# Performance work log

Hardware: AMD Instinct MI355X
Metric: run time of the kernel (lower is better)

## Reference

```python
import jax, jax.numpy as jnp
import numpy as np

GROUP_NORM_EPSILON = 1e-06
NUM_GROUPS = 32


def group_norm(x, gamma, beta, num_groups, eps):
    # x: [B, H, W, C]; normalize over (H, W, C//G) within each group.
    B, H, W, C = x.shape
    xg = x.reshape(B, H, W, num_groups, C // num_groups)
    mean = jnp.mean(xg, axis=(1, 2, 4), keepdims=True)
    var = jnp.mean(jnp.square(xg - mean), axis=(1, 2, 4), keepdims=True)
    xn = (xg - mean) * jax.lax.rsqrt(var + eps)
    return xn.reshape(B, H, W, C) * gamma + beta


def setup_inputs() -> dict:
    key = jax.random.key(0)
    ks = jax.random.split(key, 6)
    B, H, W, C = 4, 64, 64, 512
    scale = 1.0 / np.sqrt(C)
    return {
        "inputs": jax.random.normal(ks[0], (B, H, W, C), dtype=jnp.float32),
        "gamma": jnp.ones((C,), dtype=jnp.float32),
        "beta": jnp.zeros((C,), dtype=jnp.float32),
        "Wq": jax.random.normal(ks[1], (C, C), dtype=jnp.float32) * scale,
        "bq": jnp.zeros((C,), dtype=jnp.float32),
        "Wk": jax.random.normal(ks[2], (C, C), dtype=jnp.float32) * scale,
        "bk": jnp.zeros((C,), dtype=jnp.float32),
        "Wv": jax.random.normal(ks[3], (C, C), dtype=jnp.float32) * scale,
        "bv": jnp.zeros((C,), dtype=jnp.float32),
        "Wo": jax.random.normal(ks[4], (C, C), dtype=jnp.float32) * scale,
        "bo": jnp.zeros((C,), dtype=jnp.float32),
    }


def reference(inputs, gamma, beta, Wq, bq, Wk, bk, Wv, bv, Wo, bo):
    B, H, W, C = inputs.shape
    N = H * W
    h = group_norm(inputs, gamma, beta, NUM_GROUPS, GROUP_NORM_EPSILON)
    hf = h.reshape(B, N, C)  # flatten spatial: [B, N, C]
    q = hf @ Wq + bq
    k = hf @ Wk + bk
    v = hf @ Wv + bv
    # full spatial self-attention: [B, N, N]
    scores = jnp.einsum("bnc,bmc->bnm", q, k) * (C ** -0.5)
    attn = jax.nn.softmax(scores, axis=-1)
    out = jnp.einsum("bnm,bmc->bnc", attn, v)
    out = out @ Wo + bo
    return out.reshape(B, H, W, C) + inputs
```

## Files before the change

kernel.cpp:

```cpp
#include <hip/hip_runtime.h>
#include <hip/hip_bf16.h>

using bf16 = __hip_bfloat16;
using u16  = unsigned short;
typedef __attribute__((ext_vector_type(8))) short s16x8;
typedef __attribute__((ext_vector_type(4))) float f32x4;

__device__ __forceinline__ float b2f(u16 u){
  union{unsigned u; float f;} c; c.u = ((unsigned)u)<<16; return c.f;
}
__device__ __forceinline__ u16 f2b(float f){
  __hip_bfloat16 h = __float2bfloat16(f);
  return *reinterpret_cast<u16*>(&h);
}

#define GLDS16(g, l_) __builtin_amdgcn_global_load_lds( \
    (const __attribute__((address_space(1))) unsigned int*)(g), \
    (__attribute__((address_space(3))) unsigned int*)(l_), 16, 0, 0)

__global__ __launch_bounds__(512) void gn_kernel(const float* __restrict__ x,
    const float* __restrict__ gamma, const float* __restrict__ beta,
    bf16* __restrict__ h)
{
  const int b = blockIdx.x >> 5, g = blockIdx.x & 31;
  const int t = threadIdx.x;
  const size_t base = (size_t)b*4096*512 + (size_t)g*16;
  float sum = 0.f, sq = 0.f;
  for (int i = 0; i < 8; i++){
    const float* p = x + base + (size_t)(i*512 + t)*512;
    #pragma unroll
    for (int j = 0; j < 4; j++){
      f32x4 v = *(const f32x4*)(p + j*4);
      #pragma unroll
      for (int e = 0; e < 4; e++){ sum += v[e]; sq += v[e]*v[e]; }
    }
  }
  __shared__ float red[16];
  for (int o = 32; o > 0; o >>= 1){ sum += __shfl_xor(sum, o); sq += __shfl_xor(sq, o); }
  const int w = t >> 6, l = t & 63;
  if (l == 0){ red[w] = sum; red[8 + w] = sq; }
  __syncthreads();
  if (t == 0){
    float a = 0.f, bb = 0.f;
    for (int i = 0; i < 8; i++){ a += red[i]; bb += red[8 + i]; }
    red[0] = a; red[8] = bb;
  }
  __syncthreads();
  const float inv_n = 1.f/65536.f;
  const float mean = red[0]*inv_n;
  const float var  = red[8]*inv_n - mean*mean;
  const float rstd = rsqrtf(var + 1e-6f);
  float ga[16], be[16];
  #pragma unroll
  for (int j = 0; j < 16; j++){
    ga[j] = gamma[g*16 + j];
    be[j] = beta [g*16 + j];
  }
  u16* hp = (u16*)h;
  for (int i = 0; i < 8; i++){
    const float* p = x + base + (size_t)(i*512 + t)*512;
    u16* q = hp + base + (size_t)(i*512 + t)*512;
    s16x8 o0, o1;
    #pragma unroll
    for (int j = 0; j < 4; j++){
      f32x4 v = *(const f32x4*)(p + j*4);
      #pragma unroll
      for (int e = 0; e < 4; e++){
        int c = j*4 + e;
        u16 r = f2b((v[e] - mean)*rstd*ga[c] + be[c]);
        if (c < 8) o0[c] = (short)r; else o1[c - 8] = (short)r;
      }
    }
    *(s16x8*)q = o0; *(s16x8*)(q + 8) = o1;
  }
}

struct W4 { const float* p[4]; };
__global__ __launch_bounds__(256) void transpose_w4(W4 srcs, bf16* __restrict__ dst)
{
  __shared__ float tile[64][65];
  const float* in = srcs.p[blockIdx.z];
  u16* out = (u16*)dst + (size_t)blockIdx.z*512*512;
  const int tr = blockIdx.y*64, tc = blockIdx.x*64;
  const int t = threadIdx.x;
  #pragma unroll
  for (int i = 0; i < 16; i++){
    int idx = i*256 + t, r = idx >> 6, c = idx & 63;
    tile[r][c] = in[(size_t)(tr + r)*512 + tc + c];
  }
  __syncthreads();
  #pragma unroll
  for (int i = 0; i < 16; i++){
    int idx = i*256 + t, r = idx >> 6, c = idx & 63;
    out[(size_t)(tc + r)*512 + tr + c] = f2b(tile[c][r]);
  }
}

__global__ __launch_bounds__(256) void transpose_v(const u16* __restrict__ qkv,
    bf16* __restrict__ vT)
{
  __shared__ u16 tile[64][72];
  const u16* in = qkv + 1024 + (size_t)blockIdx.z*4096*1536;
  u16* out = (u16*)vT + (size_t)blockIdx.z*512*4096;
  const int tr = blockIdx.y*64, tc = blockIdx.x*64;
  const int t = threadIdx.x;
  #pragma unroll
  for (int i = 0; i < 16; i++){
    int idx = i*256 + t, r = idx >> 6, c = idx & 63;
    tile[r][c] = in[(size_t)(tr + r)*1536 + tc + c];
  }
  __syncthreads();
  #pragma unroll
  for (int i = 0; i < 16; i++){
    int idx = i*256 + t, r = idx >> 6, c = idx & 63;
    out[(size_t)(tc + r)*4096 + tr + c] = tile[c][r];
  }
}

template<int EPI, typename OutT>
__global__ __launch_bounds__(256) void gemm_bt(
    const u16* __restrict__ A, int lda, long sA,
    const u16* __restrict__ Bt, int ldb, long sB,
    OutT* __restrict__ Cmat, int ldc, long sC,
    int K, float scale,
    const float* __restrict__ b0, const float* __restrict__ b1,
    const float* __restrict__ b2, const float* __restrict__ res)
{
  __shared__ u16 As[128*64];
  __shared__ u16 Bs[128*64];
  const int t = threadIdx.x, l = t & 63, w = t >> 6;
  const int wr = w >> 1, wc = w & 1;
  int bx = blockIdx.x, by = blockIdx.y;
  {
    const int gx = gridDim.x, nb = gx * gridDim.y;
    if ((nb & 7) == 0){
      int lin = by*gx + bx;
      int s = (lin & 7)*(nb >> 3) + (lin >> 3);
      bx = s % gx; by = s / gx;
    }
  }
  const int m0 = by * 128, n0 = bx * 128;
  const u16* Au  = A  + (size_t)blockIdx.z * sA;
  const u16* Btu = Bt + (size_t)blockIdx.z * sB;

  f32x4 acc[4][4];
  #pragma unroll
  for (int m = 0; m < 4; m++)
    #pragma unroll
    for (int n = 0; n < 4; n++) acc[m][n] = (f32x4){0.f,0.f,0.f,0.f};

  const int srow = l >> 3;
  const int scol = ((l & 7) ^ srow) * 8;
  const int xorv = (l & 7) << 4;
  const int nkt = K >> 6;
  for (int kt = 0; kt < nkt; ++kt){
    const int k0 = kt << 6;
    #pragma unroll
    for (int j = 0; j < 4; j++){
      const int chunk = w*4 + j;
      const int row = chunk*8 + srow;
      GLDS16(Au  + (size_t)(m0 + row)*lda + k0 + scol, &As[chunk*512]);
      GLDS16(Btu + (size_t)(n0 + row)*ldb + k0 + scol, &Bs[chunk*512]);
    }
    __syncthreads();
    #pragma unroll
    for (int kk = 0; kk < 2; kk++){
      const int kbyte = (kk*64 + (l >> 4)*16) ^ xorv;
      s16x8 af[4], bff[4];
      #pragma unroll
      for (int m = 0; m < 4; m++)
        af[m]  = *(const s16x8*)((const char*)As + (wr*64 + m*16 + (l & 15))*128 + kbyte);
      #pragma unroll
      for (int n = 0; n < 4; n++)
        bff[n] = *(const s16x8*)((const char*)Bs + (wc*64 + n*16 + (l & 15))*128 + kbyte);
      #pragma unroll
      for (int m = 0; m < 4; m++)
        #pragma unroll
        for (int n = 0; n < 4; n++)
          acc[m][n] = __builtin_amdgcn_mfma_f32_16x16x32_bf16(af[m], bff[n], acc[m][n], 0, 0, 0);
    }
    __syncthreads();
  }
  const int lc = l & 15, lr4 = (l >> 4)*4;
  OutT* Cz = Cmat + (size_t)blockIdx.z * sC;
  #pragma unroll
  for (int n = 0; n < 4; n++){
    const int col = n0 + wc*64 + n*16 + lc;
    float bv = 0.f;
    if (EPI & 8){
      const float* bp = (col < 512) ? b0 : (col < 1024 ? b1 : b2);
      bv = bp[col & 511];
    } else if (EPI & 1){
      bv = b0[col];
    }
    #pragma unroll
    for (int m = 0; m < 4; m++){
      const int rowb = m0 + wr*64 + m*16 + lr4;
      #pragma unroll
      for (int r = 0; r < 4; r++){
        float v = acc[m][n][r];
        if (EPI & 2) v *= scale;
        v += bv;
        const size_t off = (size_t)(rowb + r)*ldc + col;
        if (EPI & 4) v += res[off];
        if constexpr (__is_same(OutT, float)) Cz[off] = v;
        else ((u16*)Cz)[off] = f2b(v);
      }
    }
  }
}

__global__ __launch_bounds__(512) void pv_fused(
    const u16* __restrict__ S, const u16* __restrict__ vT,
    bf16* __restrict__ ao, int batched, int batch0)
{
  __shared__ u16 Bs[256*64];
  __shared__ u16 Ps[64*64];
  __shared__ float lsArr[64];
  const int t = threadIdx.x, l = t & 63, w = t >> 6;
  int batch, mt, half;
  if (batched){
    const int lin = blockIdx.x, x = lin & 7, s = lin >> 3;
    batch = x >> 1; mt = (s >> 1)*2 + (x & 1); half = s & 1;
  } else { batch = batch0; mt = blockIdx.x >> 1; half = blockIdx.x & 1; }
  const int m0 = mt*64, c0 = half*256;
  const u16* Sb  = S  + (size_t)batch*4096*4096;
  const u16* vTb = vT + (size_t)batch*512*4096 + (size_t)c0*4096;
  u16* aob = (u16*)ao + (size_t)batch*4096*512;

  f32x4 acc[4][2];
  #pragma unroll
  for (int m = 0; m < 4; m++)
    #pragma unroll
    for (int n = 0; n < 2; n++) acc[m][n] = (f32x4){0.f,0.f,0.f,0.f};

  const int srow = l >> 3, lane8 = l & 7;
  const int scol = (lane8 ^ srow) * 8;
  const int xorv = lane8 << 4;
  const int r_loc = w*8 + srow;
  const int smaddr = r_loc*128 + ((lane8*16) ^ (srow << 4));
  float lsumrow = 0.f;

  const u16* Srow = Sb + (size_t)(m0 + r_loc)*4096 + lane8*8;

  #pragma unroll
  for (int j = 0; j < 4; j++){
    const int chunk = w*4 + j;
    const int row = chunk*8 + srow;
    GLDS16(vTb + (size_t)row*4096 + scol, &Bs[chunk*512]);
  }
  s16x8 S_cur = *(const s16x8*)Srow;

  for (int kt = 0; kt < 64; ++kt){
    const int ktn = (kt < 63) ? kt + 1 : 63;
    s16x8 S_next = *(const s16x8*)(Srow + ktn*64);

    float rs = 0.f;
    s16x8 pb;
    #pragma unroll
    for (int j = 0; j < 8; j++){
      const float pvv = exp2f(fminf(b2f((u16)S_cur[j]), 100.f));
      rs += pvv;
      pb[j] = (short)f2b(pvv);
    }
    rs += __shfl_xor(rs, 1); rs += __shfl_xor(rs, 2); rs += __shfl_xor(rs, 4);
    lsumrow += rs;

    *(s16x8*)((char*)Ps + smaddr) = pb;

    asm volatile("s_waitcnt lgkmcnt(0)" ::: "memory");
    __builtin_amdgcn_sched_barrier(0);
    asm volatile("s_waitcnt vmcnt(1)" ::: "memory");
    __builtin_amdgcn_sched_barrier(0);
    __builtin_amdgcn_s_barrier();

    #pragma unroll
    for (int kk = 0; kk < 2; kk++){
      const int kbyte = (kk*64 + (l >> 4)*16) ^ xorv;
      s16x8 pa[4], bf2[2];
      #pragma unroll
      for (int m = 0; m < 4; m++)
        pa[m] = *(const s16x8*)((const char*)Ps + (m*16 + (l & 15))*128 + kbyte);
      #pragma unroll
      for (int n = 0; n < 2; n++)
        bf2[n] = *(const s16x8*)((const char*)Bs + (w*32 + n*16 + (l & 15))*128 + kbyte);
      #pragma unroll
      for (int m = 0; m < 4; m++)
        #pragma unroll
        for (int n = 0; n < 2; n++)
          acc[m][n] = __builtin_amdgcn_mfma_f32_16x16x32_bf16(pa[m], bf2[n], acc[m][n], 0, 0, 0);
    }

    __builtin_amdgcn_sched_barrier(0);
    __builtin_amdgcn_s_barrier();
    __builtin_amdgcn_sched_barrier(0);

    #pragma unroll
    for (int j = 0; j < 4; j++){
      const int chunk = w*4 + j;
      const int row = chunk*8 + srow;
      GLDS16(vTb + (size_t)row*4096 + ktn*64 + scol, &Bs[chunk*512]);
    }
    S_cur = S_next;
  }

  if (lane8 == 0) lsArr[r_loc] = lsumrow;
  __syncthreads();
  #pragma unroll
  for (int m = 0; m < 4; m++){
    const f32x4 lq = *(const f32x4*)&lsArr[m*16 + (l >> 4)*4];
    #pragma unroll
    for (int r = 0; r < 4; r++){
      const float inv = 1.f / lq[r];
      const int row = m0 + m*16 + (l >> 4)*4 + r;
      #pragma unroll
      for (int n = 0; n < 2; n++){
        const int col = c0 + w*32 + n*16 + (l & 15);
        aob[(size_t)row*512 + col] = f2b(acc[m][n][r] * inv);
      }
    }
  }
}

extern "C" void kernel_launch(void* const* d_in, const int* in_sizes, int n_in,
                              void* d_out, int out_size, void* d_ws, size_t ws_size,
                              hipStream_t stream)
{
  (void)in_sizes; (void)n_in; (void)out_size;
  const float* x     = (const float*)d_in[0];
  const float* gamma = (const float*)d_in[1];
  const float* beta  = (const float*)d_in[2];
  const float* Wq = (const float*)d_in[3]; const float* bq = (const float*)d_in[4];
  const float* Wk = (const float*)d_in[5]; const float* bk = (const float*)d_in[6];
  const float* Wv = (const float*)d_in[7]; const float* bv = (const float*)d_in[8];
  const float* Wo = (const float*)d_in[9]; const float* bo = (const float*)d_in[10];
  float* out = (float*)d_out;

  const int B = 4, N = 4096, C = 512;
  const long NC = (long)N*C;
  const float scl2 = 0.04419417382415922f * 1.4426950408889634f;

  char* p0 = (char*)d_ws;
  auto align = [](size_t b){ return (b + 255) & ~(size_t)255; };
  const size_t sz_h   = align((size_t)B*NC*2);
  const size_t sz_w   = align((size_t)4*C*C*2);
  const size_t sz_qkvF= align((size_t)B*N*1536*2);
  const size_t sz_vTF = align((size_t)B*NC*2);
  const size_t sz_aoF = align((size_t)B*NC*2);
  const size_t sz_SF  = align((size_t)B*N*N*2);
  const size_t need_full = sz_h + sz_w + sz_qkvF + sz_vTF + sz_aoF + sz_SF;

  bf16* h    = (bf16*)p0;
  bf16* wAll = (bf16*)(p0 + sz_h);
  char* pv   = p0 + sz_h + sz_w;

  gn_kernel<<<dim3(B*32), dim3(512), 0, stream>>>(x, gamma, beta, h);
  W4 ws4; ws4.p[0] = Wq; ws4.p[1] = Wk; ws4.p[2] = Wv; ws4.p[3] = Wo;
  transpose_w4<<<dim3(8, 8, 4), 256, 0, stream>>>(ws4, wAll);
  bf16* woT = wAll + (size_t)3*C*C;

  if (ws_size >= need_full){
    bf16* qkv = (bf16*)pv;
    bf16* vT  = (bf16*)(pv + sz_qkvF);
    bf16* ao  = (bf16*)(pv + sz_qkvF + sz_vTF);
    bf16* S   = (bf16*)(pv + sz_qkvF + sz_vTF + sz_aoF);

    gemm_bt<8, bf16><<<dim3(12, 128, 1), 256, 0, stream>>>(
        (const u16*)h, C, 0, (const u16*)wAll, C, 0, qkv, 1536, 0,
        C, 1.f, bq, bk, bv, nullptr);
    transpose_v<<<dim3(8, 64, B), 256, 0, stream>>>((const u16*)qkv, vT);
    gemm_bt<2, bf16><<<dim3(32, 32, B), 256, 0, stream>>>(
        (const u16*)qkv, 1536, (long)N*1536, (const u16*)qkv + 512, 1536, (long)N*1536,
        S, N, (long)N*N, C, scl2, nullptr, nullptr, nullptr, nullptr);
    pv_fused<<<dim3(512), 512, 0, stream>>>(
        (const u16*)S, (const u16*)vT, ao, 1, 0);
    gemm_bt<5, float><<<dim3(4, 128, 1), 256, 0, stream>>>(
        (const u16*)ao, C, 0, (const u16*)woT, C, 0, out, C, 0,
        C, 1.f, bo, nullptr, nullptr, x);
  } else {
    const size_t sz_qkv1 = align((size_t)N*1536*2);
    const size_t sz_vT1  = align((size_t)NC*2);
    const size_t sz_ao1  = align((size_t)NC*2);
    bf16* qkv = (bf16*)pv;
    bf16* vT  = (bf16*)(pv + sz_qkv1);
    bf16* ao  = (bf16*)(pv + sz_qkv1 + sz_vT1);
    bf16* S   = (bf16*)(pv + sz_qkv1 + sz_vT1 + sz_ao1);
    for (int b = 0; b < B; b++){
      const u16* hb = (const u16*)h + (size_t)b*NC;
      gemm_bt<8, bf16><<<dim3(12, 32, 1), 256, 0, stream>>>(
          hb, C, 0, (const u16*)wAll, C, 0, qkv, 1536, 0,
          C, 1.f, bq, bk, bv, nullptr);
      transpose_v<<<dim3(8, 64, 1), 256, 0, stream>>>((const u16*)qkv, vT);
      gemm_bt<2, bf16><<<dim3(32, 32, 1), 256, 0, stream>>>(
          (const u16*)qkv, 1536, 0, (const u16*)qkv + 512, 1536, 0,
          S, N, 0, C, scl2, nullptr, nullptr, nullptr, nullptr);
      pv_fused<<<dim3(128), 512, 0, stream>>>(
          (const u16*)S, (const u16*)vT, ao, 0, b);
      gemm_bt<5, float><<<dim3(4, 32, 1), 256, 0, stream>>>(
          (const u16*)ao, C, 0, (const u16*)woT, C, 0, out + (size_t)b*NC, C, 0,
          C, 1.f, bo, nullptr, nullptr, x + (size_t)b*NC);
    }
  }
}
```

Measured before the change: 401.4 us.

## Add 256x256-tile pipelined GEMM kernel for QKV projection and QK^T scores

Adds a new gemm256 kernel that uses 512 threads and 256x256 output tiles, with double-buffered LDS staging through global_load_lds, an XOR swizzle and a phased schedule that interleaves MFMA with async loads. It also remaps block indices for L2 locality. The QKV projection and the score GEMM now use it in place of the 128-tile gemm_bt. The larger tiles aim to raise arithmetic intensity and overlap loads with compute, at the cost of higher register and LDS pressure and fewer blocks (the QKV grid shrinks to 384 blocks).

```diff
diff --git a/kernel.cpp b/kernel.cpp
--- a/kernel.cpp
+++ b/kernel.cpp
@@ -208,6 +208,141 @@
       }
     }
   }
+}
+
+template<int EPI, typename OutT>
+__global__ __launch_bounds__(512, 2) void gemm256(
+    const u16* __restrict__ A, int lda, long sA,
+    const u16* __restrict__ Bt, int ldb, long sB,
+    OutT* __restrict__ Cmat, int ldc, long sC,
+    int K, float scale,
+    const float* __restrict__ b0, const float* __restrict__ b1,
+    const float* __restrict__ b2, const float* __restrict__ res)
+{
+  __shared__ u16 L[2][2][2][256*32];
+  const int t = threadIdx.x, l = t & 63, w = t >> 3 >> 3;
+  const int wm = w >> 2, wn = w & 3;
+  int bx = blockIdx.x, by = blockIdx.y;
+  {
+    const int gx = gridDim.x, nb = gx * gridDim.y;
+    if ((nb & 7) == 0){
+      int lin = by*gx + bx;
+      int s = (lin & 7)*(nb >> 3) + (lin >> 3);
+      bx = s % gx; by = s / gx;
+    }
+  }
+  const int m0 = by * 256, n0 = bx * 256;
+  const u16* Au  = A  + (size_t)blockIdx.z * sA;
+  const u16* Btu = Bt + (size_t)blockIdx.z * sB;
+
+  f32x4 acc[8][4];
+  #pragma unroll
+  for (int m = 0; m < 8; m++)
+    #pragma unroll
+    for (int n = 0; n < 4; n++) acc[m][n] = (f32x4){0.f,0.f,0.f,0.f};
+
+  const int srow_s = t >> 2;
+  const int sce    = (((t & 3)*16) ^ (((srow_s >> 1) & 3) << 4)) >> 1;
+  const int l15 = l & 15, kb16 = (l >> 4)*16;
+
+  int arow[8], brow[4];
+  #pragma unroll
+  for (int i = 0; i < 8; i++){
+    const int r = wm*128 + i*16 + l15;
+    arow[i] = r*64 + (kb16 ^ (((r >> 1) & 3) << 4));
+  }
+  #pragma unroll
+  for (int i = 0; i < 4; i++){
+    const int r = wn*64 + i*16 + l15;
+    brow[i] = r*64 + (kb16 ^ (((r >> 1) & 3) << 4));
+  }
+
+#define STG256(HALF, XU, LD, ROW0, COLBASE) do { \
+    GLDS16((XU) + (size_t)((ROW0) + srow_s)*(LD) + (COLBASE) + sce, \
+           (char*)(HALF) + w*1024); \
+    GLDS16((XU) + (size_t)((ROW0) + 128 + srow_s)*(LD) + (COLBASE) + sce, \
+           (char*)(HALF) + 8192 + w*1024); \
+  } while(0)
+
+#define VMW4 asm volatile("s_waitcnt vmcnt(4)" ::: "memory")
+
+#define PH256(BUF, KK, MQ, STAGE_STMT, WAIT_STMT) do { \
+    s16x8 af_[4], bg_[4]; \
+    _Pragma("unroll") \
+    for (int mf = 0; mf < 4; mf++) \
+      af_[mf] = *(const s16x8*)((const char*)&L[BUF][0][KK][0] + arow[(MQ)*4 + mf]); \
+    _Pragma("unroll") \
+    for (int nf = 0; nf < 4; nf++) \
+      bg_[nf] = *(const s16x8*)((const char*)&L[BUF][1][KK][0] + brow[nf]); \
+    STAGE_STMT; \
+    WAIT_STMT; \
+    __builtin_amdgcn_s_barrier(); \
+    __builtin_amdgcn_s_setprio(1); \
+    _Pragma("unroll") \
+    for (int mf = 0; mf < 4; mf++) \
+      _Pragma("unroll") \
+      for (int nf = 0; nf < 4; nf++) \
+        acc[(MQ)*4 + mf][nf] = __builtin_amdgcn_mfma_f32_16x16x32_bf16( \
+            af_[mf], bg_[nf], acc[(MQ)*4 + mf][nf], 0, 0, 0); \
+    __builtin_amdgcn_s_setprio(0); \
+    __builtin_amdgcn_s_barrier(); \
+  } while(0)
+
+  const int nkt = K >> 6;
+  STG256(&L[0][0][0][0], Au,  lda, m0, 0);
+  STG256(&L[0][1][0][0], Btu, ldb, n0, 0);
+  STG256(&L[0][0][1][0], Au,  lda, m0, 32);
+  STG256(&L[0][1][1][0], Btu, ldb, n0, 32);
+  STG256(&L[1][0][0][0], Au,  lda, m0, 64);
+  STG256(&L[1][1][0][0], Btu, ldb, n0, 64);
+  VMW4;
+  __builtin_amdgcn_s_barrier();
+
+  const int niter = nkt >> 1;
+  for (int it = 0; it < niter; ++it){
+    const int kt1 = 2*it + 1;
+    const int kA  = (kt1 + 1 < nkt) ? kt1 + 1 : nkt - 1;
+    const int kB  = (kt1 + 2 < nkt) ? kt1 + 2 : nkt - 1;
+    PH256(0, 0, 0, STG256(&L[1][0][1][0], Au,  lda, m0, kt1*64 + 32), (void)0);
+    PH256(0, 0, 1, STG256(&L[1][1][1][0], Btu, ldb, n0, kt1*64 + 32), (void)0);
+    PH256(0, 1, 0, STG256(&L[0][0][0][0], Au,  lda, m0, kA*64),       (void)0);
+    PH256(0, 1, 1, STG256(&L[0][1][0][0], Btu, ldb, n0, kA*64),       VMW4);
+    PH256(1, 0, 0, STG256(&L[0][0][1][0], Au,  lda, m0, kA*64 + 32),  (void)0);
+    PH256(1, 0, 1, STG256(&L[0][1][1][0], Btu, ldb, n0, kA*64 + 32),  (void)0);
+    PH256(1, 1, 0, STG256(&L[1][0][0][0], Au,  lda, m0, kB*64),       (void)0);
+    PH256(1, 1, 1, STG256(&L[1][1][0][0], Btu, ldb, n0, kB*64),       VMW4);
+  }
+
+  const int lc = l15, lr4 = (l >> 4)*4;
+  OutT* Cz = Cmat + (size_t)blockIdx.z * sC;
+  #pragma unroll
+  for (int nf = 0; nf < 4; nf++){
+    const int col = n0 + wn*64 + nf*16 + lc;
+    float bv = 0.f;
+    if (EPI & 8){
+      const float* bp = (col < 512) ? b0 : (col < 1024 ? b1 : b2);
+      bv = bp[col & 511];
+    } else if (EPI & 1){
+      bv = b0[col];
+    }
+    #pragma unroll
+    for (int mf = 0; mf < 8; mf++){
+      const int rowb = m0 + wm*128 + mf*16 + lr4;
+      #pragma unroll
+      for (int r = 0; r < 4; r++){
+        float v = acc[mf][nf][r];
+        if (EPI & 2) v *= scale;
+        v += bv;
+        const size_t off = (size_t)(rowb + r)*ldc + col;
+        if (EPI & 4) v += res[off];
+        if constexpr (__is_same(OutT, float)) Cz[off] = v;
+        else ((u16*)Cz)[off] = f2b(v);
+      }
+    }
+  }
+#undef STG256
+#undef VMW4
+#undef PH256
 }
 
 __global__ __launch_bounds__(512) void pv_fused(
@@ -365,11 +500,11 @@
     bf16* ao  = (bf16*)(pv + sz_qkvF + sz_vTF);
     bf16* S   = (bf16*)(pv + sz_qkvF + sz_vTF + sz_aoF);
 
-    gemm_bt<8, bf16><<<dim3(12, 128, 1), 256, 0, stream>>>(
+    gemm256<8, bf16><<<dim3(6, 64, 1), 512, 0, stream>>>(
         (const u16*)h, C, 0, (const u16*)wAll, C, 0, qkv, 1536, 0,
         C, 1.f, bq, bk, bv, nullptr);
     transpose_v<<<dim3(8, 64, B), 256, 0, stream>>>((const u16*)qkv, vT);
-    gemm_bt<2, bf16><<<dim3(32, 32, B), 256, 0, stream>>>(
+    gemm256<2, bf16><<<dim3(16, 16, B), 512, 0, stream>>>(
         (const u16*)qkv, 1536, (long)N*1536, (const u16*)qkv + 512, 1536, (long)N*1536,
         S, N, (long)N*N, C, scl2, nullptr, nullptr, nullptr, nullptr);
     pv_fused<<<dim3(512), 512, 0, stream>>>(
@@ -387,11 +522,11 @@
     bf16* S   = (bf16*)(pv + sz_qkv1 + sz_vT1 + sz_ao1);
     for (int b = 0; b < B; b++){
       const u16* hb = (const u16*)h + (size_t)b*NC;
-      gemm_bt<8, bf16><<<dim3(12, 32, 1), 256, 0, stream>>>(
+      gemm256<8, bf16><<<dim3(6, 16, 1), 512, 0, stream>>>(
           hb, C, 0, (const u16*)wAll, C, 0, qkv, 1536, 0,
           C, 1.f, bq, bk, bv, nullptr);
       transpose_v<<<dim3(8, 64, 1), 256, 0, stream>>>((const u16*)qkv, vT);
-      gemm_bt<2, bf16><<<dim3(32, 32, 1), 256, 0, stream>>>(
+      gemm256<2, bf16><<<dim3(16, 16, 1), 512, 0, stream>>>(
           (const u16*)qkv, 1536, 0, (const u16*)qkv + 512, 1536, 0,
           S, N, 0, C, scl2, nullptr, nullptr, nullptr, nullptr);
       pv_fused<<<dim3(128), 512, 0, stream>>>(
```

New measurement: 424.6 us. +5.8%, slower.
